# Kernel optimization log

Hardware: AMD Instinct MI355X
Metric: run time of the kernel (lower is better)

The kernel has to match this reference:

```python
import jax, jax.numpy as jnp
import numpy as np

BRANCH = [True, False] * 10  # branchLs: joints that also emit a tracking frame
TRACK_IDX = np.where(np.array(BRANCH))[0]


def rpy2r(rpy):
    # rpy (..., 3) -> rotation (..., 3, 3), R = Rz(yaw) @ Ry(pitch) @ Rx(roll)
    r, p, y = rpy[..., 0], rpy[..., 1], rpy[..., 2]
    cr, sr = jnp.cos(r), jnp.sin(r)
    cp, sp = jnp.cos(p), jnp.sin(p)
    cy, sy = jnp.cos(y), jnp.sin(y)
    return jnp.stack([
        jnp.stack([cy * cp, cy * sp * sr - sy * cr, cy * sp * cr + sy * sr], -1),
        jnp.stack([sy * cp, sy * sp * sr + cy * cr, sy * sp * cr - cy * sr], -1),
        jnp.stack([-sp, cp * sr, cp * cr], -1)], -2)


def pr2t(p, R):
    # p (...,3), R (...,3,3) -> homogeneous transform (...,4,4)
    top = jnp.concatenate([R, p[..., None]], axis=-1)
    bot = jnp.broadcast_to(jnp.array([0., 0., 0., 1.], R.dtype), top.shape[:-2] + (1, 4))
    return jnp.concatenate([top, bot], axis=-2)


def rodrigues(axis, q):
    # axis (J,3) (normalized inside), q (B,J) angles -> (B,J,3,3)
    a = axis / (jnp.linalg.norm(axis, axis=-1, keepdims=True) + 1e-12)
    ax, ay, az = a[..., 0], a[..., 1], a[..., 2]
    z = jnp.zeros_like(ax)
    K = jnp.stack([jnp.stack([z, -az, ay], -1),
                   jnp.stack([az, z, -ax], -1),
                   jnp.stack([-ay, ax, z], -1)], -2)  # (J,3,3)
    K2 = K @ K
    s = jnp.sin(q)[..., None, None]  # (B,J,1,1)
    c = jnp.cos(q)[..., None, None]
    return jnp.eye(3, dtype=q.dtype) + s * K + (1. - c) * K2


def _forward(rev_q, pri_q, rev_p_off, rev_rpy_off, pri_p_off, pri_rpy_off,
             rev_axis, pri_axis, p_track, rpy_track):
    B, J = rev_q.shape
    dt = rev_q.dtype
    rev_T_off = pr2t(rev_p_off, rpy2r(rev_rpy_off))    # (J,4,4)
    pri_T_off = pr2t(pri_p_off, rpy2r(pri_rpy_off))    # (J,4,4)
    T_track = pr2t(p_track, rpy2r(rpy_track))          # (J,4,4)
    rev_T = pr2t(jnp.zeros((B, J, 3), dt), rodrigues(rev_axis, rev_q))  # (B,J,4,4)
    eye3 = jnp.broadcast_to(jnp.eye(3, dtype=dt), (B, J, 3, 3))
    pri_T = pr2t(pri_q[..., None] * pri_axis[None], eye3)               # (B,J,4,4)
    # fold constant offsets into per-joint steps, joint axis leading for scan
    rev_step = jnp.einsum('jab,njbc->jnac', rev_T_off, rev_T)  # (J,B,4,4)
    pri_step = jnp.einsum('jab,njbc->jnac', pri_T_off, pri_T)  # (J,B,4,4)

    def step(out, xs):
        rs, ps, tt = xs
        out1 = out @ rs          # after revolute joint
        out2 = out1 @ ps         # after prismatic joint
        return out2, (out1, out2, out2 @ tt)

    init = jnp.broadcast_to(jnp.eye(4, dtype=dt), (B, 4, 4))
    _, (rev_all, pri_all, trk_all) = jax.lax.scan(step, init, (rev_step, pri_step, T_track))
    RevSE3 = jnp.transpose(rev_all, (1, 0, 2, 3))                  # (B,J,4,4)
    PriSE3 = jnp.transpose(pri_all, (1, 0, 2, 3))                  # (B,J,4,4)
    TrackingSE3 = jnp.transpose(trk_all[TRACK_IDX], (1, 0, 2, 3))  # (B,n_track,4,4)
    return TrackingSE3, RevSE3, PriSE3


def setup_inputs() -> dict:
    key = jax.random.key(0)
    ks = jax.random.split(key, 10)
    B, J = 32768, 20
    u = lambda k, s: jax.random.uniform(k, s, jnp.float32, -1., 1.)
    return {
        'rev_q_value': jax.random.normal(ks[0], (B, J), jnp.float32),
        'pri_q_value': jax.random.normal(ks[1], (B, J), jnp.float32),
        'rev_p_offset': u(ks[2], (J, 3)), 'rev_rpy_offset': u(ks[3], (J, 3)),
        'pri_p_offset': u(ks[4], (J, 3)), 'pri_rpy_offset': u(ks[5], (J, 3)),
        'rev_axis': u(ks[6], (J, 3)), 'pri_axis': u(ks[7], (J, 3)),
        'p_track': u(ks[8], (J, 3)), 'rpy_track': u(ks[9], (J, 3)),
    }


def reference(rev_q_value, pri_q_value, rev_p_offset, rev_rpy_offset,
              pri_p_offset, pri_rpy_offset, rev_axis, pri_axis, p_track, rpy_track):
    return _forward(rev_q_value, pri_q_value, rev_p_offset, rev_rpy_offset,
                    pri_p_offset, pri_rpy_offset, rev_axis, pri_axis, p_track, rpy_track)
```

## Files before the change

kernel.cpp:

```cpp
#include <hip/hip_runtime.h>
#include <math.h>


constexpr int NJ  = 20;
constexpr int GB  = 8;
constexpr int BSTR = 151;
constexpr int PRIO = 60;
constexpr int TRKO = 120;

typedef float v4f __attribute__((ext_vector_type(4)));

struct Aff { float R[9]; float p[3]; };

__device__ __forceinline__ void rpy2r_dev(float r, float p, float y, float R[9]) {
    float sr, cr, sp, cp, sy, cy;
    __sincosf(r, &sr, &cr);
    __sincosf(p, &sp, &cp);
    __sincosf(y, &sy, &cy);
    R[0] = cy * cp; R[1] = cy * sp * sr - sy * cr; R[2] = cy * sp * cr + sy * sr;
    R[3] = sy * cp; R[4] = sy * sp * sr + cy * cr; R[5] = sy * sp * cr - cy * sr;
    R[6] = -sp;     R[7] = cp * sr;                R[8] = cp * cr;
}

__device__ __forceinline__ void mat33_mul(const float A[9], const float B[9], float C[9]) {
#pragma unroll
    for (int i = 0; i < 3; ++i) {
        C[3 * i + 0] = A[3 * i + 0] * B[0] + A[3 * i + 1] * B[3] + A[3 * i + 2] * B[6];
        C[3 * i + 1] = A[3 * i + 0] * B[1] + A[3 * i + 1] * B[4] + A[3 * i + 2] * B[7];
        C[3 * i + 2] = A[3 * i + 0] * B[2] + A[3 * i + 1] * B[5] + A[3 * i + 2] * B[8];
    }
}

__device__ __forceinline__ Aff compose(const Aff& A, const Aff& B) {
    Aff C;
    mat33_mul(A.R, B.R, C.R);
#pragma unroll
    for (int i = 0; i < 3; ++i)
        C.p[i] = fmaf(A.R[3 * i + 0], B.p[0],
                 fmaf(A.R[3 * i + 1], B.p[1],
                 fmaf(A.R[3 * i + 2], B.p[2], A.p[i])));
    return C;
}

__device__ __forceinline__ Aff shfl_up_aff(const Aff& V, int d) {
    Aff N;
#pragma unroll
    for (int k = 0; k < 9; ++k) N.R[k] = __shfl_up(V.R[k], d, 32);
#pragma unroll
    for (int k = 0; k < 3; ++k) N.p[k] = __shfl_up(V.p[k], d, 32);
    return N;
}

__global__ __launch_bounds__(256) void fk_kernel(
    const float* __restrict__ rev_q,      const float* __restrict__ pri_q,
    const float* __restrict__ rev_p_off,  const float* __restrict__ rev_rpy_off,
    const float* __restrict__ pri_p_off,  const float* __restrict__ pri_rpy_off,
    const float* __restrict__ rev_axis,   const float* __restrict__ pri_axis,
    const float* __restrict__ p_track,    const float* __restrict__ rpy_track,
    float* __restrict__ out, int B)
{
    __shared__ float4 cst[NJ][11];
    __shared__ v4f stg[GB * BSTR];
    const int t = threadIdx.x;

    if (t < NJ) {
        const int j = t;
        float Ro[9], Rp[9], Rt[9];
        rpy2r_dev(rev_rpy_off[3 * j], rev_rpy_off[3 * j + 1], rev_rpy_off[3 * j + 2], Ro);
        rpy2r_dev(pri_rpy_off[3 * j], pri_rpy_off[3 * j + 1], pri_rpy_off[3 * j + 2], Rp);
        rpy2r_dev(rpy_track[3 * j],   rpy_track[3 * j + 1],   rpy_track[3 * j + 2],   Rt);
        cst[j][0] = make_float4(Ro[0], Ro[1], Ro[2], rev_p_off[3 * j + 0]);
        cst[j][1] = make_float4(Ro[3], Ro[4], Ro[5], rev_p_off[3 * j + 1]);
        cst[j][2] = make_float4(Ro[6], Ro[7], Ro[8], rev_p_off[3 * j + 2]);
        cst[j][3] = make_float4(Rp[0], Rp[1], Rp[2], pri_p_off[3 * j + 0]);
        cst[j][4] = make_float4(Rp[3], Rp[4], Rp[5], pri_p_off[3 * j + 1]);
        cst[j][5] = make_float4(Rp[6], Rp[7], Rp[8], pri_p_off[3 * j + 2]);
        cst[j][6] = make_float4(Rt[0], Rt[1], Rt[2], p_track[3 * j + 0]);
        cst[j][7] = make_float4(Rt[3], Rt[4], Rt[5], p_track[3 * j + 1]);
        cst[j][8] = make_float4(Rt[6], Rt[7], Rt[8], p_track[3 * j + 2]);
        const float ax = rev_axis[3 * j], ay = rev_axis[3 * j + 1], az = rev_axis[3 * j + 2];
        const float inv = 1.0f / (sqrtf(ax * ax + ay * ay + az * az) + 1e-12f);
        cst[j][9] = make_float4(ax * inv, ay * inv, az * inv, 0.0f);
        const float px = pri_axis[3 * j], py = pri_axis[3 * j + 1], pz = pri_axis[3 * j + 2];
        cst[j][10] = make_float4(Rp[0] * px + Rp[1] * py + Rp[2] * pz,
                                 Rp[3] * px + Rp[4] * py + Rp[5] * pz,
                                 Rp[6] * px + Rp[7] * py + Rp[8] * pz, 0.0f);
    }
    __syncthreads();

    const int j = t & 31;
    const int g = t >> 5;
    const int b = blockIdx.x * GB + g;

    if (j < NJ) {
        const float rq = rev_q[(size_t)b * NJ + j];
        const float pq = pri_q[(size_t)b * NJ + j];

        float s, c;
        __sincosf(rq, &s, &c);
        const float4 a4 = cst[j][9];
        const float ax = a4.x, ay = a4.y, az = a4.z, omc = 1.0f - c;
        float Rr[9];
        Rr[0] = c + omc * ax * ax;      Rr[1] = omc * ax * ay - s * az; Rr[2] = omc * ax * az + s * ay;
        Rr[3] = omc * ax * ay + s * az; Rr[4] = c + omc * ay * ay;      Rr[5] = omc * ay * az - s * ax;
        Rr[6] = omc * ax * az - s * ay; Rr[7] = omc * ay * az + s * ax; Rr[8] = c + omc * az * az;

        const float4 cr0 = cst[j][0], cr1 = cst[j][1], cr2 = cst[j][2];
        const float Roff[9] = {cr0.x, cr0.y, cr0.z, cr1.x, cr1.y, cr1.z, cr2.x, cr2.y, cr2.z};
        Aff revstep;
        mat33_mul(Roff, Rr, revstep.R);
        revstep.p[0] = cr0.w; revstep.p[1] = cr1.w; revstep.p[2] = cr2.w;

        const float4 cp0 = cst[j][3], cp1 = cst[j][4], cp2 = cst[j][5];
        const float4 w4 = cst[j][10];
        const float Rpoff[9] = {cp0.x, cp0.y, cp0.z, cp1.x, cp1.y, cp1.z, cp2.x, cp2.y, cp2.z};
        const float pp[3] = {fmaf(pq, w4.x, cp0.w), fmaf(pq, w4.y, cp1.w), fmaf(pq, w4.z, cp2.w)};

        Aff V;
        mat33_mul(revstep.R, Rpoff, V.R);
#pragma unroll
        for (int i = 0; i < 3; ++i)
            V.p[i] = fmaf(revstep.R[3 * i + 0], pp[0],
                     fmaf(revstep.R[3 * i + 1], pp[1],
                     fmaf(revstep.R[3 * i + 2], pp[2], revstep.p[i])));

#pragma unroll
        for (int d = 1; d < 32; d <<= 1) {
            Aff N = shfl_up_aff(V, d);
            if (j >= d) V = compose(N, V);
        }

        Aff P = shfl_up_aff(V, 1);
        if (j == 0) {
            P.R[0] = 1.f; P.R[1] = 0.f; P.R[2] = 0.f;
            P.R[3] = 0.f; P.R[4] = 1.f; P.R[5] = 0.f;
            P.R[6] = 0.f; P.R[7] = 0.f; P.R[8] = 1.f;
            P.p[0] = 0.f; P.p[1] = 0.f; P.p[2] = 0.f;
        }
        const Aff Rev = compose(P, revstep);

        v4f* sg = &stg[g * BSTR];
        sg[3 * j + 0] = (v4f){Rev.R[0], Rev.R[1], Rev.R[2], Rev.p[0]};
        sg[3 * j + 1] = (v4f){Rev.R[3], Rev.R[4], Rev.R[5], Rev.p[1]};
        sg[3 * j + 2] = (v4f){Rev.R[6], Rev.R[7], Rev.R[8], Rev.p[2]};
        sg[PRIO + 3 * j + 0] = (v4f){V.R[0], V.R[1], V.R[2], V.p[0]};
        sg[PRIO + 3 * j + 1] = (v4f){V.R[3], V.R[4], V.R[5], V.p[1]};
        sg[PRIO + 3 * j + 2] = (v4f){V.R[6], V.R[7], V.R[8], V.p[2]};

        if ((j & 1) == 0) {
            const float4 ct0 = cst[j][6], ct1 = cst[j][7], ct2 = cst[j][8];
            Aff T;
            T.R[0] = ct0.x; T.R[1] = ct0.y; T.R[2] = ct0.z;
            T.R[3] = ct1.x; T.R[4] = ct1.y; T.R[5] = ct1.z;
            T.R[6] = ct2.x; T.R[7] = ct2.y; T.R[8] = ct2.z;
            T.p[0] = ct0.w; T.p[1] = ct1.w; T.p[2] = ct2.w;
            const Aff Trk = compose(V, T);
            const int jt = j >> 1;
            sg[TRKO + 3 * jt + 0] = (v4f){Trk.R[0], Trk.R[1], Trk.R[2], Trk.p[0]};
            sg[TRKO + 3 * jt + 1] = (v4f){Trk.R[3], Trk.R[4], Trk.R[5], Trk.p[1]};
            sg[TRKO + 3 * jt + 2] = (v4f){Trk.R[6], Trk.R[7], Trk.R[8], Trk.p[2]};
        }
    }
    __syncthreads();

    v4f* out4 = reinterpret_cast<v4f*>(out);
    const v4f bot = (v4f){0.f, 0.f, 0.f, 1.f};
    const int blockBase = blockIdx.x * GB;

    {
        v4f* dst = out4 + (size_t)blockBase * 40;
#pragma unroll
        for (int k = t; k < GB * 40; k += 256) {
            const int gg = k / 40, w = k - gg * 40;
            const int jt = w >> 2, r = w & 3;
            const v4f v = (r == 3) ? bot : stg[gg * BSTR + TRKO + 3 * jt + r];
            __builtin_nontemporal_store(v, &dst[k]);
        }
    }
    {
        v4f* dst = out4 + (size_t)B * 40 + (size_t)blockBase * 80;
#pragma unroll
        for (int k = t; k < GB * 80; k += 256) {
            const int gg = k / 80, w = k - gg * 80;
            const int jj = w >> 2, r = w & 3;
            const v4f v = (r == 3) ? bot : stg[gg * BSTR + 3 * jj + r];
            __builtin_nontemporal_store(v, &dst[k]);
        }
    }
    {
        v4f* dst = out4 + (size_t)B * 120 + (size_t)blockBase * 80;
#pragma unroll
        for (int k = t; k < GB * 80; k += 256) {
            const int gg = k / 80, w = k - gg * 80;
            const int jj = w >> 2, r = w & 3;
            const v4f v = (r == 3) ? bot : stg[gg * BSTR + PRIO + 3 * jj + r];
            __builtin_nontemporal_store(v, &dst[k]);
        }
    }
}

extern "C" void kernel_launch(void* const* d_in, const int* in_sizes, int n_in,
                              void* d_out, int out_size, void* d_ws, size_t ws_size,
                              hipStream_t stream) {
    (void)n_in; (void)out_size; (void)d_ws; (void)ws_size;
    const float* rev_q       = (const float*)d_in[0];
    const float* pri_q       = (const float*)d_in[1];
    const float* rev_p_off   = (const float*)d_in[2];
    const float* rev_rpy_off = (const float*)d_in[3];
    const float* pri_p_off   = (const float*)d_in[4];
    const float* pri_rpy_off = (const float*)d_in[5];
    const float* rev_axis    = (const float*)d_in[6];
    const float* pri_axis    = (const float*)d_in[7];
    const float* p_track     = (const float*)d_in[8];
    const float* rpy_track   = (const float*)d_in[9];

    const int B = in_sizes[0] / NJ;
    const int blocks = B / GB;
    fk_kernel<<<dim3(blocks), dim3(256), 0, stream>>>(
        rev_q, pri_q, rev_p_off, rev_rpy_off, pri_p_off, pri_rpy_off,
        rev_axis, pri_axis, p_track, rpy_track, (float*)d_out, B);
}
```

Baseline: 139.2 us.

## Pack two joints per lane, scan over 16-lane rows with DPP, drop block barrier

Each lane now handles two consecutive joints, so a batch item occupies 16 lanes instead of 32, and each block covers twice as many batch items. The prefix scan of rigid transforms runs in four steps using DPP row-shift instructions instead of five shuffle steps. The second __syncthreads is replaced by having each wavefront write only the batch items it computed itself. This aims to cut idle lanes, shuffle cost and barrier stalls, at the cost of more register pressure per lane and a dependence on DPP row semantics.

```diff
diff --git a/kernel.cpp b/kernel.cpp
--- a/kernel.cpp
+++ b/kernel.cpp
@@ -2,11 +2,11 @@
 #include <math.h>
 
 
-constexpr int NJ  = 20;
-constexpr int GB  = 8;
-constexpr int BSTR = 151;
-constexpr int PRIO = 60;
-constexpr int TRKO = 120;
+constexpr int NJ    = 20;
+constexpr int GBATCH = 16;
+constexpr int BSTR  = 151;
+constexpr int PRIO  = 60;
+constexpr int TRKO  = 120;
 
 typedef float v4f __attribute__((ext_vector_type(4)));
 
@@ -42,13 +42,55 @@
     return C;
 }
 
-__device__ __forceinline__ Aff shfl_up_aff(const Aff& V, int d) {
+template <int D>
+__device__ __forceinline__ float dpp_shr(float x) {
+    constexpr int CTRL = 0x110 | D;
+    return __int_as_float(__builtin_amdgcn_update_dpp(
+        0, __float_as_int(x), CTRL, 0xF, 0xF, true));
+}
+
+template <int D>
+__device__ __forceinline__ Aff dpp_up(const Aff& V) {
     Aff N;
 #pragma unroll
-    for (int k = 0; k < 9; ++k) N.R[k] = __shfl_up(V.R[k], d, 32);
-#pragma unroll
-    for (int k = 0; k < 3; ++k) N.p[k] = __shfl_up(V.p[k], d, 32);
+    for (int k = 0; k < 9; ++k) N.R[k] = dpp_shr<D>(V.R[k]);
+#pragma unroll
+    for (int k = 0; k < 3; ++k) N.p[k] = dpp_shr<D>(V.p[k]);
     return N;
+}
+
+__device__ __forceinline__ void joint_step(const float4 cst[11], float rq, float pq,
+                                           Aff& revstep, Aff& S) {
+    float s, c;
+    __sincosf(rq, &s, &c);
+    const float4 a4 = cst[9];
+    const float ax = a4.x, ay = a4.y, az = a4.z, omc = 1.0f - c;
+    float Rr[9];
+    Rr[0] = c + omc * ax * ax;      Rr[1] = omc * ax * ay - s * az; Rr[2] = omc * ax * az + s * ay;
+    Rr[3] = omc * ax * ay + s * az; Rr[4] = c + omc * ay * ay;      Rr[5] = omc * ay * az - s * ax;
+    Rr[6] = omc * ax * az - s * ay; Rr[7] = omc * ay * az + s * ax; Rr[8] = c + omc * az * az;
+
+    const float4 cr0 = cst[0], cr1 = cst[1], cr2 = cst[2];
+    const float Roff[9] = {cr0.x, cr0.y, cr0.z, cr1.x, cr1.y, cr1.z, cr2.x, cr2.y, cr2.z};
+    mat33_mul(Roff, Rr, revstep.R);
+    revstep.p[0] = cr0.w; revstep.p[1] = cr1.w; revstep.p[2] = cr2.w;
+
+    const float4 cp0 = cst[3], cp1 = cst[4], cp2 = cst[5];
+    const float4 w4 = cst[10];
+    const float Rpoff[9] = {cp0.x, cp0.y, cp0.z, cp1.x, cp1.y, cp1.z, cp2.x, cp2.y, cp2.z};
+    const float pp[3] = {fmaf(pq, w4.x, cp0.w), fmaf(pq, w4.y, cp1.w), fmaf(pq, w4.z, cp2.w)};
+    mat33_mul(revstep.R, Rpoff, S.R);
+#pragma unroll
+    for (int i = 0; i < 3; ++i)
+        S.p[i] = fmaf(revstep.R[3 * i + 0], pp[0],
+                 fmaf(revstep.R[3 * i + 1], pp[1],
+                 fmaf(revstep.R[3 * i + 2], pp[2], revstep.p[i])));
+}
+
+__device__ __forceinline__ void stage3(v4f* sg, int base, const Aff& A) {
+    sg[base + 0] = (v4f){A.R[0], A.R[1], A.R[2], A.p[0]};
+    sg[base + 1] = (v4f){A.R[3], A.R[4], A.R[5], A.p[1]};
+    sg[base + 2] = (v4f){A.R[6], A.R[7], A.R[8], A.p[2]};
 }
 
 __global__ __launch_bounds__(256) void fk_kernel(
@@ -60,7 +102,7 @@
     float* __restrict__ out, int B)
 {
     __shared__ float4 cst[NJ][11];
-    __shared__ v4f stg[GB * BSTR];
+    __shared__ v4f stg[GBATCH * BSTR];
     const int t = threadIdx.x;
 
     if (t < NJ) {
@@ -88,112 +130,91 @@
     }
     __syncthreads();
 
-    const int j = t & 31;
-    const int g = t >> 5;
-    const int b = blockIdx.x * GB + g;
-
-    if (j < NJ) {
-        const float rq = rev_q[(size_t)b * NJ + j];
-        const float pq = pri_q[(size_t)b * NJ + j];
-
-        float s, c;
-        __sincosf(rq, &s, &c);
-        const float4 a4 = cst[j][9];
-        const float ax = a4.x, ay = a4.y, az = a4.z, omc = 1.0f - c;
-        float Rr[9];
-        Rr[0] = c + omc * ax * ax;      Rr[1] = omc * ax * ay - s * az; Rr[2] = omc * ax * az + s * ay;
-        Rr[3] = omc * ax * ay + s * az; Rr[4] = c + omc * ay * ay;      Rr[5] = omc * ay * az - s * ax;
-        Rr[6] = omc * ax * az - s * ay; Rr[7] = omc * ay * az + s * ax; Rr[8] = c + omc * az * az;
-
-        const float4 cr0 = cst[j][0], cr1 = cst[j][1], cr2 = cst[j][2];
-        const float Roff[9] = {cr0.x, cr0.y, cr0.z, cr1.x, cr1.y, cr1.z, cr2.x, cr2.y, cr2.z};
-        Aff revstep;
-        mat33_mul(Roff, Rr, revstep.R);
-        revstep.p[0] = cr0.w; revstep.p[1] = cr1.w; revstep.p[2] = cr2.w;
-
-        const float4 cp0 = cst[j][3], cp1 = cst[j][4], cp2 = cst[j][5];
-        const float4 w4 = cst[j][10];
-        const float Rpoff[9] = {cp0.x, cp0.y, cp0.z, cp1.x, cp1.y, cp1.z, cp2.x, cp2.y, cp2.z};
-        const float pp[3] = {fmaf(pq, w4.x, cp0.w), fmaf(pq, w4.y, cp1.w), fmaf(pq, w4.z, cp2.w)};
-
-        Aff V;
-        mat33_mul(revstep.R, Rpoff, V.R);
-#pragma unroll
-        for (int i = 0; i < 3; ++i)
-            V.p[i] = fmaf(revstep.R[3 * i + 0], pp[0],
-                     fmaf(revstep.R[3 * i + 1], pp[1],
-                     fmaf(revstep.R[3 * i + 2], pp[2], revstep.p[i])));
-
-#pragma unroll
-        for (int d = 1; d < 32; d <<= 1) {
-            Aff N = shfl_up_aff(V, d);
-            if (j >= d) V = compose(N, V);
-        }
-
-        Aff P = shfl_up_aff(V, 1);
-        if (j == 0) {
-            P.R[0] = 1.f; P.R[1] = 0.f; P.R[2] = 0.f;
-            P.R[3] = 0.f; P.R[4] = 1.f; P.R[5] = 0.f;
-            P.R[6] = 0.f; P.R[7] = 0.f; P.R[8] = 1.f;
-            P.p[0] = 0.f; P.p[1] = 0.f; P.p[2] = 0.f;
-        }
-        const Aff Rev = compose(P, revstep);
+    const int l = t & 15;
+    const int g = t >> 4;
+    const int b = blockIdx.x * GBATCH + g;
+
+    if (l < 10) {
+        const int j0 = 2 * l, j1 = 2 * l + 1;
+        const float rq0 = rev_q[(size_t)b * NJ + j0];
+        const float rq1 = rev_q[(size_t)b * NJ + j1];
+        const float pq0 = pri_q[(size_t)b * NJ + j0];
+        const float pq1 = pri_q[(size_t)b * NJ + j1];
+
+        Aff rs0, S0, rs1, S1;
+        joint_step(cst[j0], rq0, pq0, rs0, S0);
+        joint_step(cst[j1], rq1, pq1, rs1, S1);
+
+        Aff V = compose(S0, S1);
+
+        { Aff N = dpp_up<1>(V); if (l >= 1) V = compose(N, V); }
+        { Aff N = dpp_up<2>(V); if (l >= 2) V = compose(N, V); }
+        { Aff N = dpp_up<4>(V); if (l >= 4) V = compose(N, V); }
+        { Aff N = dpp_up<8>(V); if (l >= 8) V = compose(N, V); }
+
+        Aff E = dpp_up<1>(V);
+        if (l == 0) {
+            E.R[0] = 1.f; E.R[1] = 0.f; E.R[2] = 0.f;
+            E.R[3] = 0.f; E.R[4] = 1.f; E.R[5] = 0.f;
+            E.R[6] = 0.f; E.R[7] = 0.f; E.R[8] = 1.f;
+            E.p[0] = 0.f; E.p[1] = 0.f; E.p[2] = 0.f;
+        }
+
+        const Aff rev0 = compose(E, rs0);
+        const Aff T0   = compose(E, S0);
+        const Aff rev1 = compose(T0, rs1);
 
         v4f* sg = &stg[g * BSTR];
-        sg[3 * j + 0] = (v4f){Rev.R[0], Rev.R[1], Rev.R[2], Rev.p[0]};
-        sg[3 * j + 1] = (v4f){Rev.R[3], Rev.R[4], Rev.R[5], Rev.p[1]};
-        sg[3 * j + 2] = (v4f){Rev.R[6], Rev.R[7], Rev.R[8], Rev.p[2]};
-        sg[PRIO + 3 * j + 0] = (v4f){V.R[0], V.R[1], V.R[2], V.p[0]};
-        sg[PRIO + 3 * j + 1] = (v4f){V.R[3], V.R[4], V.R[5], V.p[1]};
-        sg[PRIO + 3 * j + 2] = (v4f){V.R[6], V.R[7], V.R[8], V.p[2]};
-
-        if ((j & 1) == 0) {
-            const float4 ct0 = cst[j][6], ct1 = cst[j][7], ct2 = cst[j][8];
-            Aff T;
-            T.R[0] = ct0.x; T.R[1] = ct0.y; T.R[2] = ct0.z;
-            T.R[3] = ct1.x; T.R[4] = ct1.y; T.R[5] = ct1.z;
-            T.R[6] = ct2.x; T.R[7] = ct2.y; T.R[8] = ct2.z;
-            T.p[0] = ct0.w; T.p[1] = ct1.w; T.p[2] = ct2.w;
-            const Aff Trk = compose(V, T);
-            const int jt = j >> 1;
-            sg[TRKO + 3 * jt + 0] = (v4f){Trk.R[0], Trk.R[1], Trk.R[2], Trk.p[0]};
-            sg[TRKO + 3 * jt + 1] = (v4f){Trk.R[3], Trk.R[4], Trk.R[5], Trk.p[1]};
-            sg[TRKO + 3 * jt + 2] = (v4f){Trk.R[6], Trk.R[7], Trk.R[8], Trk.p[2]};
-        }
-    }
-    __syncthreads();
+        stage3(sg, 3 * j0, rev0);
+        stage3(sg, 3 * j1, rev1);
+        stage3(sg, PRIO + 3 * j0, T0);
+        stage3(sg, PRIO + 3 * j1, V);
+
+        {
+            const float4 ct0 = cst[j0][6], ct1 = cst[j0][7], ct2 = cst[j0][8];
+            Aff Tt;
+            Tt.R[0] = ct0.x; Tt.R[1] = ct0.y; Tt.R[2] = ct0.z;
+            Tt.R[3] = ct1.x; Tt.R[4] = ct1.y; Tt.R[5] = ct1.z;
+            Tt.R[6] = ct2.x; Tt.R[7] = ct2.y; Tt.R[8] = ct2.z;
+            Tt.p[0] = ct0.w; Tt.p[1] = ct1.w; Tt.p[2] = ct2.w;
+            const Aff Trk = compose(T0, Tt);
+            stage3(sg, TRKO + 3 * l, Trk);
+        }
+    }
 
     v4f* out4 = reinterpret_cast<v4f*>(out);
     const v4f bot = (v4f){0.f, 0.f, 0.f, 1.f};
-    const int blockBase = blockIdx.x * GB;
+    const int w = t >> 6, lw = t & 63;
+    const int gbase = 4 * w;
+    const size_t batch0 = (size_t)blockIdx.x * GBATCH + gbase;
 
     {
-        v4f* dst = out4 + (size_t)blockBase * 40;
-#pragma unroll
-        for (int k = t; k < GB * 40; k += 256) {
-            const int gg = k / 40, w = k - gg * 40;
-            const int jt = w >> 2, r = w & 3;
-            const v4f v = (r == 3) ? bot : stg[gg * BSTR + TRKO + 3 * jt + r];
+        v4f* dst = out4 + batch0 * 40;
+#pragma unroll
+        for (int k = lw; k < 160; k += 64) {
+            const int gg = k / 40, ww = k - gg * 40;
+            const int jt = ww >> 2, r = ww & 3;
+            const v4f v = (r == 3) ? bot : stg[(gbase + gg) * BSTR + TRKO + 3 * jt + r];
             __builtin_nontemporal_store(v, &dst[k]);
         }
     }
     {
-        v4f* dst = out4 + (size_t)B * 40 + (size_t)blockBase * 80;
-#pragma unroll
-        for (int k = t; k < GB * 80; k += 256) {
-            const int gg = k / 80, w = k - gg * 80;
-            const int jj = w >> 2, r = w & 3;
-            const v4f v = (r == 3) ? bot : stg[gg * BSTR + 3 * jj + r];
+        v4f* dst = out4 + (size_t)B * 40 + batch0 * 80;
+#pragma unroll
+        for (int k = lw; k < 320; k += 64) {
+            const int gg = k / 80, ww = k - gg * 80;
+            const int jj = ww >> 2, r = ww & 3;
+            const v4f v = (r == 3) ? bot : stg[(gbase + gg) * BSTR + 3 * jj + r];
             __builtin_nontemporal_store(v, &dst[k]);
         }
     }
     {
-        v4f* dst = out4 + (size_t)B * 120 + (size_t)blockBase * 80;
-#pragma unroll
-        for (int k = t; k < GB * 80; k += 256) {
-            const int gg = k / 80, w = k - gg * 80;
-            const int jj = w >> 2, r = w & 3;
-            const v4f v = (r == 3) ? bot : stg[gg * BSTR + PRIO + 3 * jj + r];
+        v4f* dst = out4 + (size_t)B * 120 + batch0 * 80;
+#pragma unroll
+        for (int k = lw; k < 320; k += 64) {
+            const int gg = k / 80, ww = k - gg * 80;
+            const int jj = ww >> 2, r = ww & 3;
+            const v4f v = (r == 3) ? bot : stg[(gbase + gg) * BSTR + PRIO + 3 * jj + r];
             __builtin_nontemporal_store(v, &dst[k]);
         }
     }
@@ -215,7 +236,7 @@
     const float* rpy_track   = (const float*)d_in[9];
 
     const int B = in_sizes[0] / NJ;
-    const int blocks = B / GB;
+    const int blocks = B / GBATCH;
     fk_kernel<<<dim3(blocks), dim3(256), 0, stream>>>(
         rev_q, pri_q, rev_p_off, rev_rpy_off, pri_p_off, pri_rpy_off,
         rev_axis, pri_axis, p_track, rpy_track, (float*)d_out, B);
```

After: 184.8 us. 1.33x slower.
